# Kernel optimization log

Hardware: AMD Instinct MI355X
Metric: run time of the kernel (lower is better)

Reference implementation:

```python
import jax, jax.numpy as jnp
import numpy as np

B_, S, D = 2, 2048, 2048
F_ = 8192
R = 16
H = 16
HD = D // H
MOD_SCALE = 0.1
EPS = 1e-6


def _rmsnorm(x, w):
    v = jnp.mean(x * x, axis=-1, keepdims=True)
    return x * jax.lax.rsqrt(v + EPS) * w


def setup_inputs() -> dict:
    key = jax.random.key(0)
    ks = jax.random.split(key, 12)
    sd = 0.02
    return {
        "hidden_states": jax.random.normal(ks[0], (B_, S, D), jnp.float32),
        "ln1_w": jnp.ones((D,), jnp.float32),
        "ln2_w": jnp.ones((D,), jnp.float32),
        "Wq": jax.random.normal(ks[1], (D, D), jnp.float32) * sd,
        "Wk": jax.random.normal(ks[2], (D, D), jnp.float32) * sd,
        "Wv": jax.random.normal(ks[3], (D, D), jnp.float32) * sd,
        "Wo": jax.random.normal(ks[4], (D, D), jnp.float32) * sd,
        "A": jax.random.normal(ks[5], (D, R), jnp.float32) * (0.01 / np.sqrt(D)),
        "B": jax.random.normal(ks[6], (R, F_), jnp.float32) * (0.01 / np.sqrt(R)),
        "W_in_base": jax.random.normal(ks[7], (F_, D), jnp.float32) * sd,
        "W_up_base": jax.random.normal(ks[8], (F_, D), jnp.float32) * sd,
        "W_down": jax.random.normal(ks[9], (D, F_), jnp.float32) * sd,
    }


def _attention(x, Wq, Wk, Wv, Wo):
    # x: (b, s, d). Causal multi-head self-attention, torch Linear convention (y = x @ W.T).
    b, s, d = x.shape
    q = (x @ Wq.T).reshape(b, s, H, HD)
    k = (x @ Wk.T).reshape(b, s, H, HD)
    v = (x @ Wv.T).reshape(b, s, H, HD)
    scores = jnp.einsum("bqhd,bkhd->bhqk", q, k) / np.sqrt(HD).astype(np.float32)
    causal = jnp.tril(jnp.ones((s, s), bool))
    scores = jnp.where(causal, scores, jnp.finfo(scores.dtype).min)
    probs = jax.nn.softmax(scores, axis=-1)
    out = jnp.einsum("bhqk,bkhd->bqhd", probs, v).reshape(b, s, d)
    return out @ Wo.T


def reference(hidden_states, ln1_w, ln2_w, Wq, Wk, Wv, Wo, A, B, W_in_base, W_up_base, W_down):
    residual = hidden_states
    x = _rmsnorm(hidden_states, ln1_w)
    attn = _attention(x, Wq, Wk, Wv, Wo)  # (b, s, d)

    # NeuroPlasticComponent: delta_w[b,s,d,f] = sum_r mod[b,s,r] * A[d,r] * B[r,f]
    mod = MOD_SCALE * jnp.tanh(attn @ A)  # (b, s, r)

    # NPT quirk: post_attention_layernorm is applied to the ORIGINAL residual,
    # and attention output is never added into the residual stream.
    h = _rmsnorm(residual, ln2_w)  # (b, s, d)

    # Per-token modulated gate: (W_in_base + delta_w[b,s].T) @ h
    # delta_w[b,s].T @ h = sum_d delta[d,f] h[d] = ((mod * (h @ A)) @ B)[f]
    gate_pre = h @ W_in_base.T + (mod * (h @ A)) @ B  # (b, s, f)
    gate = jax.nn.silu(gate_pre)
    up = h @ W_up_base.T
    mlp_out = (gate * up) @ W_down.T
    return residual + mlp_out
```

## Files before the change

### kernel.cpp

```cpp
#include <hip/hip_runtime.h>

#define DI __device__ __forceinline__

typedef short s16x8 __attribute__((ext_vector_type(8)));
typedef float f32x4 __attribute__((ext_vector_type(4)));

typedef __attribute__((address_space(1))) const unsigned int as1_cuint;
typedef __attribute__((address_space(3))) unsigned int as3_uint;

DI unsigned short f2bf(float f) {
  union { float f; unsigned int u; } v; v.f = f;
  unsigned int r = v.u + 0x7fffu + ((v.u >> 16) & 1u);
  return (unsigned short)(r >> 16);
}
DI float bf2f(unsigned short b) {
  union { unsigned int u; float f; } v; v.u = ((unsigned int)b) << 16;
  return v.f;
}

DI void gl_lds16(const void* g, void* l) {
  __builtin_amdgcn_global_load_lds((as1_cuint*)g, (as3_uint*)l, 16, 0, 0);
}

DI void bar() {
  __builtin_amdgcn_sched_barrier(0);
  __builtin_amdgcn_s_barrier();
  __builtin_amdgcn_sched_barrier(0);
}
DI void s_vmcnt6() { asm volatile("s_waitcnt vmcnt(6)" ::: "memory"); }
DI void s_vmcnt0() { asm volatile("s_waitcnt vmcnt(0)" ::: "memory"); }

DI void stage_half(const unsigned short* gb, size_t r0, int K, int kt,
                   unsigned short* lh, int tid) {
#pragma unroll
  for (int j = 0; j < 2; ++j) {
    int o = j * 8192 + tid * 16;
    int row = o >> 7, cb = o & 127;
    int scb = cb ^ ((row & 7) << 4);
    gl_lds16(gb + (r0 + row) * (size_t)K + kt + (scb >> 1),
             lh + ((j * 8192 + (tid >> 6) * 1024) >> 1));
  }
}

DI s16x8 rd_frag(const unsigned short* lds, int baseE, int rwh, int kh, int lane) {
  int cb = kh * 64 + ((lane >> 4) << 4);
  int scb = cb ^ ((rwh & 7) << 4);
  return *(const s16x8*)&lds[baseE + rwh * 64 + (scb >> 1)];
}

__global__ __launch_bounds__(256) void cvt_f32_bf16(const float* __restrict__ src,
                                                    unsigned short* __restrict__ dst, int n4) {
  int i = blockIdx.x * blockDim.x + threadIdx.x;
  int stride = gridDim.x * blockDim.x;
  for (; i < n4; i += stride) {
    float4 v = ((const float4*)src)[i];
    ((ushort4*)dst)[i] = make_ushort4(f2bf(v.x), f2bf(v.y), f2bf(v.z), f2bf(v.w));
  }
}

__global__ __launch_bounds__(256) void rmsnorm_dual(const float* __restrict__ hs,
                                                    const float* __restrict__ w1,
                                                    const float* __restrict__ w2,
                                                    unsigned short* __restrict__ xo,
                                                    unsigned short* __restrict__ ho) {
  const int D = 2048;
  int t = blockIdx.x, tid = threadIdx.x;
  const float* row = hs + (size_t)t * D;
  float4 a = ((const float4*)row)[tid * 2];
  float4 b = ((const float4*)row)[tid * 2 + 1];
  float ss = a.x * a.x + a.y * a.y + a.z * a.z + a.w * a.w +
             b.x * b.x + b.y * b.y + b.z * b.z + b.w * b.w;
#pragma unroll
  for (int off = 32; off; off >>= 1) ss += __shfl_xor(ss, off);
  __shared__ float red[4];
  int wave = tid >> 6, lane = tid & 63;
  if (lane == 0) red[wave] = ss;
  __syncthreads();
  float tot = red[0] + red[1] + red[2] + red[3];
  float inv = rsqrtf(tot / (float)D + 1e-6f);
  int base = tid * 8;
  float vals[8] = {a.x, a.y, a.z, a.w, b.x, b.y, b.z, b.w};
  float4 w1a = ((const float4*)(w1 + base))[0];
  float4 w1b = ((const float4*)(w1 + base))[1];
  float4 w2a = ((const float4*)(w2 + base))[0];
  float4 w2b = ((const float4*)(w2 + base))[1];
  float w1v[8] = {w1a.x, w1a.y, w1a.z, w1a.w, w1b.x, w1b.y, w1b.z, w1b.w};
  float w2v[8] = {w2a.x, w2a.y, w2a.z, w2a.w, w2b.x, w2b.y, w2b.z, w2b.w};
  unsigned short ox[8], oh[8];
#pragma unroll
  for (int j = 0; j < 8; ++j) {
    float n = vals[j] * inv;
    ox[j] = f2bf(n * w1v[j]);
    oh[j] = f2bf(n * w2v[j]);
  }
  ushort4* xp = (ushort4*)(xo + (size_t)t * D + base);
  ushort4* hp = (ushort4*)(ho + (size_t)t * D + base);
  xp[0] = make_ushort4(ox[0], ox[1], ox[2], ox[3]);
  xp[1] = make_ushort4(ox[4], ox[5], ox[6], ox[7]);
  hp[0] = make_ushort4(oh[0], oh[1], oh[2], oh[3]);
  hp[1] = make_ushort4(oh[4], oh[5], oh[6], oh[7]);
}

#define E_NONE 0
#define E_RES 3

template <int EPI>
__global__ __launch_bounds__(512, 2) void gemm256(
    const unsigned short* __restrict__ Amat, const unsigned short* __restrict__ Bt,
    int N, int K, unsigned short* __restrict__ Cbf, float* __restrict__ Cf,
    const float* __restrict__ Res) {
  __shared__ __align__(16) unsigned short lds[65536];
  int tid = threadIdx.x, lane = tid & 63;
  int w = tid >> 6, wm = w >> 2, wn = w & 3;
  int lr = lane & 15, lkh = lane >> 4;
  int nbn = N >> 8, nwg = gridDim.x, wg = blockIdx.x;
  int cpx = nwg >> 3;
  int swz = (wg & 7) * cpx + (wg >> 3);
  int tm = swz / nbn, tn = swz - tm * nbn;
  size_t m0 = (size_t)tm * 256, n0 = (size_t)tn * 256;
  int NT = K >> 6;

  auto stage = [&](int tau, int slot) {
    if (tau >= NT) return;
    const unsigned short* gb = (slot >= 2) ? Bt : Amat;
    size_t r0 = (slot >= 2) ? (n0 + (size_t)(slot - 2) * 128) : (m0 + (size_t)slot * 128);
    stage_half(gb, r0, K, tau * 64, &lds[(tau & 1) * 32768 + slot * 8192], tid);
  };

  stage(0, 0); stage(0, 2); stage(0, 1); stage(0, 3);
  stage(1, 0); stage(1, 2); stage(1, 1);
  s_vmcnt6();
  bar();

  f32x4 acc[8][4] = {};
  s16x8 afr[4][2], bfr[2][2][2];

  for (int t = 0; t < NT; ++t) {
    int buf = (t & 1) * 32768;
#pragma unroll
    for (int mi = 0; mi < 4; ++mi)
#pragma unroll
      for (int kh = 0; kh < 2; ++kh)
        afr[mi][kh] = rd_frag(lds, buf + 0 * 8192, mi * 32 + wm * 16 + lr, kh, lane);
#pragma unroll
    for (int ni = 0; ni < 2; ++ni)
#pragma unroll
      for (int kh = 0; kh < 2; ++kh)
        bfr[0][ni][kh] = rd_frag(lds, buf + 2 * 8192, ni * 64 + wn * 16 + lr, kh, lane);
    stage(t + 1, 3);
    bar();
    __builtin_amdgcn_s_setprio(1);
#pragma unroll
    for (int mi = 0; mi < 4; ++mi)
#pragma unroll
      for (int ni = 0; ni < 2; ++ni)
#pragma unroll
        for (int kh = 0; kh < 2; ++kh)
          acc[mi][ni] = __builtin_amdgcn_mfma_f32_16x16x32_bf16(afr[mi][kh], bfr[0][ni][kh], acc[mi][ni], 0, 0, 0);
    __builtin_amdgcn_s_setprio(0);
    bar();
#pragma unroll
    for (int ni = 0; ni < 2; ++ni)
#pragma unroll
      for (int kh = 0; kh < 2; ++kh)
        bfr[1][ni][kh] = rd_frag(lds, buf + 3 * 8192, ni * 64 + wn * 16 + lr, kh, lane);
    stage(t + 2, 0);
    bar();
    __builtin_amdgcn_s_setprio(1);
#pragma unroll
    for (int mi = 0; mi < 4; ++mi)
#pragma unroll
      for (int ni = 0; ni < 2; ++ni)
#pragma unroll
        for (int kh = 0; kh < 2; ++kh)
          acc[mi][2 + ni] = __builtin_amdgcn_mfma_f32_16x16x32_bf16(afr[mi][kh], bfr[1][ni][kh], acc[mi][2 + ni], 0, 0, 0);
    __builtin_amdgcn_s_setprio(0);
    bar();
#pragma unroll
    for (int mi = 0; mi < 4; ++mi)
#pragma unroll
      for (int kh = 0; kh < 2; ++kh)
        afr[mi][kh] = rd_frag(lds, buf + 1 * 8192, mi * 32 + wm * 16 + lr, kh, lane);
    stage(t + 2, 2);
    bar();
    __builtin_amdgcn_s_setprio(1);
#pragma unroll
    for (int mi = 0; mi < 4; ++mi)
#pragma unroll
      for (int ni = 0; ni < 2; ++ni)
#pragma unroll
        for (int kh = 0; kh < 2; ++kh)
          acc[4 + mi][ni] = __builtin_amdgcn_mfma_f32_16x16x32_bf16(afr[mi][kh], bfr[0][ni][kh], acc[4 + mi][ni], 0, 0, 0);
    __builtin_amdgcn_s_setprio(0);
    bar();
    stage(t + 2, 1);
    bar();
    __builtin_amdgcn_s_setprio(1);
#pragma unroll
    for (int mi = 0; mi < 4; ++mi)
#pragma unroll
      for (int ni = 0; ni < 2; ++ni)
#pragma unroll
        for (int kh = 0; kh < 2; ++kh)
          acc[4 + mi][2 + ni] = __builtin_amdgcn_mfma_f32_16x16x32_bf16(afr[mi][kh], bfr[1][ni][kh], acc[4 + mi][2 + ni], 0, 0, 0);
    __builtin_amdgcn_s_setprio(0);
    if (t < NT - 2) s_vmcnt6();
    else if (t == NT - 2) s_vmcnt0();
    bar();
  }

#pragma unroll
  for (int mh = 0; mh < 2; ++mh)
#pragma unroll
    for (int mi = 0; mi < 4; ++mi)
#pragma unroll
      for (int r = 0; r < 4; ++r) {
        size_t row = m0 + mh * 128 + mi * 32 + wm * 16 + lkh * 4 + r;
#pragma unroll
        for (int nh = 0; nh < 2; ++nh)
#pragma unroll
          for (int ni = 0; ni < 2; ++ni) {
            size_t col = n0 + nh * 128 + ni * 64 + wn * 16 + lr;
            float v = acc[mh * 4 + mi][nh * 2 + ni][r];
            if constexpr (EPI == E_RES) Cf[row * N + col] = Res[row * N + col] + v;
            else Cbf[row * N + col] = f2bf(v);
          }
      }
}

__global__ __launch_bounds__(512, 2) void gemm_mlp256(
    const unsigned short* __restrict__ Hm, const unsigned short* __restrict__ Wg,
    const unsigned short* __restrict__ Wu,
    const float* __restrict__ cvec, const float* __restrict__ Bsm,
    unsigned short* __restrict__ Out) {
  const int N = 8192, K = 2048, NT = K >> 6;
  __shared__ __align__(16) unsigned short lds[65536];
  int tid = threadIdx.x, lane = tid & 63;
  int w = tid >> 6, wm = w >> 2, wn = w & 3;
  int lr = lane & 15, lkh = lane >> 4;
  int nbn = N >> 7, nwg = gridDim.x, wg = blockIdx.x;
  int cpx = nwg >> 3;
  int swz = (wg & 7) * cpx + (wg >> 3);
  int tm = swz / nbn, tn = swz - tm * nbn;
  size_t m0 = (size_t)tm * 256, n0 = (size_t)tn * 128;

  auto stage = [&](int tau, int slot) {
    if (tau >= NT) return;
    const unsigned short* gb = (slot == 2) ? Wg : (slot == 3) ? Wu : Hm;
    size_t r0 = (slot >= 2) ? n0 : (m0 + (size_t)slot * 128);
    stage_half(gb, r0, K, tau * 64, &lds[(tau & 1) * 32768 + slot * 8192], tid);
  };

  stage(0, 0); stage(0, 2); stage(0, 1); stage(0, 3);
  stage(1, 0); stage(1, 2); stage(1, 1);
  s_vmcnt6();
  bar();

  f32x4 ag[8][2] = {}, au[8][2] = {};
  s16x8 afr[4][2], bg[2][2], bu[2][2];

  for (int t = 0; t < NT; ++t) {
    int buf = (t & 1) * 32768;
#pragma unroll
    for (int mi = 0; mi < 4; ++mi)
#pragma unroll
      for (int kh = 0; kh < 2; ++kh)
        afr[mi][kh] = rd_frag(lds, buf + 0 * 8192, mi * 32 + wm * 16 + lr, kh, lane);
#pragma unroll
    for (int ni = 0; ni < 2; ++ni)
#pragma unroll
      for (int kh = 0; kh < 2; ++kh)
        bg[ni][kh] = rd_frag(lds, buf + 2 * 8192, ni * 64 + wn * 16 + lr, kh, lane);
    stage(t + 1, 3);
    bar();
    __builtin_amdgcn_s_setprio(1);
#pragma unroll
    for (int mi = 0; mi < 4; ++mi)
#pragma unroll
      for (int ni = 0; ni < 2; ++ni)
#pragma unroll
        for (int kh = 0; kh < 2; ++kh)
          ag[mi][ni] = __builtin_amdgcn_mfma_f32_16x16x32_bf16(afr[mi][kh], bg[ni][kh], ag[mi][ni], 0, 0, 0);
    __builtin_amdgcn_s_setprio(0);
    bar();
#pragma unroll
    for (int ni = 0; ni < 2; ++ni)
#pragma unroll
      for (int kh = 0; kh < 2; ++kh)
        bu[ni][kh] = rd_frag(lds, buf + 3 * 8192, ni * 64 + wn * 16 + lr, kh, lane);
    stage(t + 2, 0);
    bar();
    __builtin_amdgcn_s_setprio(1);
#pragma unroll
    for (int mi = 0; mi < 4; ++mi)
#pragma unroll
      for (int ni = 0; ni < 2; ++ni)
#pragma unroll
        for (int kh = 0; kh < 2; ++kh)
          au[mi][ni] = __builtin_amdgcn_mfma_f32_16x16x32_bf16(afr[mi][kh], bu[ni][kh], au[mi][ni], 0, 0, 0);
    __builtin_amdgcn_s_setprio(0);
    bar();
#pragma unroll
    for (int mi = 0; mi < 4; ++mi)
#pragma unroll
      for (int kh = 0; kh < 2; ++kh)
        afr[mi][kh] = rd_frag(lds, buf + 1 * 8192, mi * 32 + wm * 16 + lr, kh, lane);
    stage(t + 2, 2);
    bar();
    __builtin_amdgcn_s_setprio(1);
#pragma unroll
    for (int mi = 0; mi < 4; ++mi)
#pragma unroll
      for (int ni = 0; ni < 2; ++ni)
#pragma unroll
        for (int kh = 0; kh < 2; ++kh)
          ag[4 + mi][ni] = __builtin_amdgcn_mfma_f32_16x16x32_bf16(afr[mi][kh], bg[ni][kh], ag[4 + mi][ni], 0, 0, 0);
    __builtin_amdgcn_s_setprio(0);
    bar();
    stage(t + 2, 1);
    bar();
    __builtin_amdgcn_s_setprio(1);
#pragma unroll
    for (int mi = 0; mi < 4; ++mi)
#pragma unroll
      for (int ni = 0; ni < 2; ++ni)
#pragma unroll
        for (int kh = 0; kh < 2; ++kh)
          au[4 + mi][ni] = __builtin_amdgcn_mfma_f32_16x16x32_bf16(afr[mi][kh], bu[ni][kh], au[4 + mi][ni], 0, 0, 0);
    __builtin_amdgcn_s_setprio(0);
    if (t < NT - 2) s_vmcnt6();
    else if (t == NT - 2) s_vmcnt0();
    bar();
  }

  float* cl = (float*)lds;
  float* bl = (float*)&lds[32768];
#pragma unroll
  for (int j = 0; j < 2; ++j) {
    int fi = tid * 2 + j;
    ((float4*)cl)[fi] = ((const float4*)(cvec + m0 * 16))[fi];
  }
  {
    int fi = tid;
    ((float4*)bl)[fi] = *(const float4*)(Bsm + (size_t)(fi >> 5) * N + n0 + (fi & 31) * 4);
  }
  bar();

#pragma unroll
  for (int mh = 0; mh < 2; ++mh)
#pragma unroll
    for (int mi = 0; mi < 4; ++mi)
#pragma unroll
      for (int r = 0; r < 4; ++r) {
        int rr = mh * 128 + mi * 32 + wm * 16 + lkh * 4 + r;
        size_t row = m0 + rr;
#pragma unroll
        for (int ni = 0; ni < 2; ++ni) {
          int cc = ni * 64 + wn * 16 + lr;
          size_t col = n0 + cc;
          float s = 0.f;
#pragma unroll
          for (int jj = 0; jj < 16; ++jj) s += cl[rr * 16 + jj] * bl[jj * 128 + cc];
          float g = ag[mh * 4 + mi][ni][r] + s;
          float sig = 1.f / (1.f + __expf(-g));
          Out[row * N + col] = f2bf(g * sig * au[mh * 4 + mi][ni][r]);
        }
      }
}

__global__ __launch_bounds__(256) void vtrans(const unsigned short* __restrict__ qkv,
                                              unsigned short* __restrict__ vT) {
  __shared__ unsigned short t[64][72];
  int bh = blockIdx.z, b = bh >> 4, h = bh & 15;
  int k0 = blockIdx.x * 64, d0 = blockIdx.y * 64;
  int tid = threadIdx.x;
#pragma unroll
  for (int j = 0; j < 2; ++j) {
    int idx = tid + j * 256;
    int r = idx >> 3, c8 = (idx & 7) * 8;
    s16x8 v = *(const s16x8*)(qkv + ((size_t)(b * 2048 + k0 + r)) * 6144 + 4096 + h * 128 + d0 + c8);
#pragma unroll
    for (int e = 0; e < 8; ++e) t[r][c8 + e] = (unsigned short)v[e];
  }
  __syncthreads();
#pragma unroll
  for (int j = 0; j < 2; ++j) {
    int idx = tid + j * 256;
    int dr = idx >> 3, k8 = (idx & 7) * 8;
    s16x8 o;
#pragma unroll
    for (int e = 0; e < 8; ++e) o[e] = (short)t[k8 + e][dr];
    *(s16x8*)(vT + (size_t)bh * 262144 + (size_t)(d0 + dr) * 2048 + k0 + k8) = o;
  }
}

__global__ __launch_bounds__(256, 2) void attn_fwd2(const unsigned short* __restrict__ qkv,
                                                    const unsigned short* __restrict__ vT,
                                                    unsigned short* __restrict__ attn) {
  const int LD = 6144;
  __shared__ __align__(16) unsigned short Kt[8192];
  __shared__ __align__(16) unsigned short Vt[8192];
  __shared__ __align__(16) unsigned short Pl[4096];
  int tid = threadIdx.x, w = tid >> 6, lane = tid & 63;
  int lrow = lane & 15, g = lane >> 4;
  int qp = blockIdx.x, bh = blockIdx.y, b = bh >> 4, h = bh & 15;
  const unsigned short* Qb = qkv + (size_t)b * 2048 * LD + h * 128;
  const unsigned short* Kb = Qb + 2048;
  const unsigned short* vTb = vT + (size_t)bh * 262144;
  const float scale = 0.08838834764831845f;

#pragma unroll
  for (int pass = 0; pass < 2; ++pass) {
    int qtile = pass ? (31 - qp) : qp;
    int wq0 = qtile * 64 + w * 16;
    s16x8 qf[4];
#pragma unroll
    for (int kc = 0; kc < 4; ++kc)
      qf[kc] = *(const s16x8*)(Qb + (size_t)(wq0 + lrow) * LD + kc * 32 + g * 8);
    f32x4 ao[8] = {};
    float m_r[4], l_r[4];
#pragma unroll
    for (int r = 0; r < 4; ++r) { m_r[r] = -1e30f; l_r[r] = 0.f; }
    int nkt = qtile + 1;

    for (int kt = 0; kt < nkt; ++kt) {
      int k0 = kt * 64;
      bar();
#pragma unroll
      for (int j = 0; j < 4; ++j) {
        int o = j * 4096 + tid * 16;
        int row = o >> 8, cb = o & 255;
        int scb = cb ^ ((row & 7) << 4);
        gl_lds16(Kb + (size_t)(k0 + row) * LD + (scb >> 1), &Kt[(j * 4096 + w * 1024) >> 1]);
      }
#pragma unroll
      for (int j = 0; j < 4; ++j) {
        int o = j * 4096 + tid * 16;
        int row = o >> 7, cb = o & 127;
        int scb = cb ^ ((row & 7) << 4);
        gl_lds16(vTb + (size_t)row * 2048 + k0 + (scb >> 1), &Vt[(j * 4096 + w * 1024) >> 1]);
      }
      s_vmcnt0();
      bar();
      f32x4 sa[4] = {};
#pragma unroll
      for (int ni = 0; ni < 4; ++ni)
#pragma unroll
        for (int kc = 0; kc < 4; ++kc) {
          int row = ni * 16 + lrow;
          int cb = kc * 64 + g * 16;
          int scb = cb ^ ((row & 7) << 4);
          s16x8 kf = *(const s16x8*)&Kt[row * 128 + (scb >> 1)];
          sa[ni] = __builtin_amdgcn_mfma_f32_16x16x32_bf16(qf[kc], kf, sa[ni], 0, 0, 0);
        }
      if (k0 + 63 > wq0) {
#pragma unroll
        for (int ni = 0; ni < 4; ++ni)
#pragma unroll
          for (int r = 0; r < 4; ++r) {
            int q_idx = wq0 + g * 4 + r, k_idx = k0 + ni * 16 + lrow;
            float sv = sa[ni][r] * scale;
            sa[ni][r] = (k_idx > q_idx) ? -1e30f : sv;
          }
      } else {
#pragma unroll
        for (int ni = 0; ni < 4; ++ni)
#pragma unroll
          for (int r = 0; r < 4; ++r) sa[ni][r] *= scale;
      }
      float mt[4];
#pragma unroll
      for (int r = 0; r < 4; ++r)
        mt[r] = fmaxf(fmaxf(sa[0][r], sa[1][r]), fmaxf(sa[2][r], sa[3][r]));
#pragma unroll
      for (int r = 0; r < 4; ++r)
#pragma unroll
        for (int off = 8; off; off >>= 1) mt[r] = fmaxf(mt[r], __shfl_xor(mt[r], off));
      float al[4];
#pragma unroll
      for (int r = 0; r < 4; ++r) {
        float mn = fmaxf(m_r[r], mt[r]);
        al[r] = __expf(m_r[r] - mn);
        m_r[r] = mn;
      }
      float rs[4] = {0.f, 0.f, 0.f, 0.f};
#pragma unroll
      for (int ni = 0; ni < 4; ++ni)
#pragma unroll
        for (int r = 0; r < 4; ++r) {
          float p = __expf(sa[ni][r] - m_r[r]);
          rs[r] += p;
          int q = g * 4 + r, k = ni * 16 + lrow;
          Pl[w * 1024 + q * 64 + (k ^ ((q & 7) << 3))] = f2bf(p);
        }
#pragma unroll
      for (int r = 0; r < 4; ++r) {
#pragma unroll
        for (int off = 8; off; off >>= 1) rs[r] += __shfl_xor(rs[r], off);
        l_r[r] = l_r[r] * al[r] + rs[r];
      }
#pragma unroll
      for (int df = 0; df < 8; ++df)
#pragma unroll
        for (int r = 0; r < 4; ++r) ao[df][r] *= al[r];
      asm volatile("s_waitcnt lgkmcnt(0)" ::: "memory");
      __builtin_amdgcn_sched_barrier(0);
      s16x8 pa[2];
#pragma unroll
      for (int ks = 0; ks < 2; ++ks)
        pa[ks] = *(const s16x8*)&Pl[w * 1024 + lrow * 64 + ((ks * 32 + g * 8) ^ ((lrow & 7) << 3))];
#pragma unroll
      for (int df = 0; df < 8; ++df) {
#pragma unroll
        for (int ks = 0; ks < 2; ++ks) {
          int row = df * 16 + lrow;
          int cb = ks * 64 + g * 16;
          int scb = cb ^ ((row & 7) << 4);
          s16x8 vf = *(const s16x8*)&Vt[row * 64 + (scb >> 1)];
          ao[df] = __builtin_amdgcn_mfma_f32_16x16x32_bf16(pa[ks], vf, ao[df], 0, 0, 0);
        }
      }
    }
#pragma unroll
    for (int df = 0; df < 8; ++df)
#pragma unroll
      for (int r = 0; r < 4; ++r) {
        int q = wq0 + g * 4 + r;
        float v = ao[df][r] / l_r[r];
        attn[((size_t)b * 2048 + q) * 2048 + h * 128 + df * 16 + lrow] = f2bf(v);
      }
    bar();
  }
}

__global__ __launch_bounds__(256) void modc(const unsigned short* __restrict__ attnO,
                                            const unsigned short* __restrict__ h,
                                            const float* __restrict__ A,
                                            float* __restrict__ cvec) {
  const int D = 2048;
  int t = blockIdx.x * 4 + (threadIdx.x >> 6);
  int lane = threadIdx.x & 63;
  float aA[16] = {}, aH[16] = {};
  for (int i = 0; i < D / 64; ++i) {
    int d = i * 64 + lane;
    float av = bf2f(attnO[(size_t)t * D + d]);
    float hv = bf2f(h[(size_t)t * D + d]);
    const float* ar = A + (size_t)d * 16;
#pragma unroll
    for (int j = 0; j < 16; ++j) {
      float a = ar[j];
      aA[j] += av * a;
      aH[j] += hv * a;
    }
  }
#pragma unroll
  for (int j = 0; j < 16; ++j) {
#pragma unroll
    for (int off = 32; off; off >>= 1) {
      aA[j] += __shfl_xor(aA[j], off);
      aH[j] += __shfl_xor(aH[j], off);
    }
  }
#pragma unroll
  for (int j = 0; j < 16; ++j)
    if (lane == j) cvec[(size_t)t * 16 + j] = 0.1f * tanhf(aA[j]) * aH[j];
}

extern "C" void kernel_launch(void* const* d_in, const int* in_sizes, int n_in,
                              void* d_out, int out_size, void* d_ws, size_t ws_size,
                              hipStream_t stream) {
  const float* hs  = (const float*)d_in[0];
  const float* ln1 = (const float*)d_in[1];
  const float* ln2 = (const float*)d_in[2];
  const float* Wq  = (const float*)d_in[3];
  const float* Wk  = (const float*)d_in[4];
  const float* Wv  = (const float*)d_in[5];
  const float* Wo  = (const float*)d_in[6];
  const float* Am  = (const float*)d_in[7];
  const float* Bm  = (const float*)d_in[8];
  const float* Win = (const float*)d_in[9];
  const float* Wup = (const float*)d_in[10];
  const float* Wdn = (const float*)d_in[11];
  float* out = (float*)d_out;
  (void)in_sizes; (void)n_in;

  const int T = 4096;
  const int Dm = 2048, F = 8192;
  const size_t MB = (size_t)1 << 20;

  const size_t need = 184 * MB;
  if (ws_size < need) {
    hipMemsetAsync(d_out, 0, (size_t)out_size * 4, stream);
    return;
  }
  char* base = (char*)d_ws;
  unsigned short* tb    = (unsigned short*)(base);
  unsigned short* wqkv  = (unsigned short*)(base);
  unsigned short* vT    = (unsigned short*)(base);
  unsigned short* xb    = (unsigned short*)(base + 24 * MB);
  unsigned short* attnO = (unsigned short*)(base + 40 * MB);
  unsigned short* qkv   = (unsigned short*)(base + 64 * MB);
  unsigned short* win   = (unsigned short*)(base + 64 * MB);
  unsigned short* wo    = (unsigned short*)(base + 112 * MB);
  unsigned short* hb    = (unsigned short*)(base + 120 * MB);
  unsigned short* attn  = (unsigned short*)(base + 136 * MB);
  float*          cv    = (float*)(base + 136 * MB);
  unsigned short* wup   = (unsigned short*)(base + 152 * MB);
  unsigned short* wdn   = (unsigned short*)(base + 152 * MB);

  cvt_f32_bf16<<<2048, 256, 0, stream>>>(Wq, wqkv, Dm * Dm / 4);
  cvt_f32_bf16<<<2048, 256, 0, stream>>>(Wk, wqkv + (size_t)Dm * Dm, Dm * Dm / 4);
  cvt_f32_bf16<<<2048, 256, 0, stream>>>(Wv, wqkv + (size_t)2 * Dm * Dm, Dm * Dm / 4);
  cvt_f32_bf16<<<2048, 256, 0, stream>>>(Wo, wo, Dm * Dm / 4);
  rmsnorm_dual<<<T, 256, 0, stream>>>(hs, ln1, ln2, xb, hb);

  gemm256<E_NONE><<<(T / 256) * (3 * Dm / 256), 512, 0, stream>>>(
      xb, wqkv, 3 * Dm, Dm, qkv, nullptr, nullptr);

  vtrans<<<dim3(32, 2, 32), 256, 0, stream>>>(qkv, vT);

  attn_fwd2<<<dim3(16, 32), 256, 0, stream>>>(qkv, vT, attn);

  gemm256<E_NONE><<<(T / 256) * (Dm / 256), 512, 0, stream>>>(
      attn, wo, Dm, Dm, attnO, nullptr, nullptr);

  modc<<<T / 4, 256, 0, stream>>>(attnO, hb, Am, cv);

  cvt_f32_bf16<<<2048, 256, 0, stream>>>(Win, win, F * Dm / 4);
  cvt_f32_bf16<<<2048, 256, 0, stream>>>(Wup, wup, F * Dm / 4);

  gemm_mlp256<<<(T / 256) * (F / 128), 512, 0, stream>>>(hb, win, wup, cv, Bm, tb);

  cvt_f32_bf16<<<2048, 256, 0, stream>>>(Wdn, wdn, Dm * F / 4);
  gemm256<E_RES><<<(T / 256) * (Dm / 256), 512, 0, stream>>>(
      tb, wdn, Dm, F, nullptr, out, hs);
}
```

Before: 905.7 us.

## Switch GEMMs to 256x128 tiles with precomputed LDS offsets and one-stage prefetch

Replaces the 256x256 general GEMM with a 256x128-tile variant, which doubles the workgroup count for the QKV, O-projection and down-projection GEMMs (T=4096 rows). Both the general GEMM and the fused MLP GEMM now precompute swizzled LDS fragment offsets and staging pointers once, instead of recomputing addresses every tile. Both pipelines change from staging two K-tiles ahead to a double-buffered one-tile-ahead prefetch, with fewer barriers per iteration. The smaller tiles lower arithmetic intensity per workgroup, and the shallower prefetch may expose more global-load latency.

```diff
diff --git a/kernel.cpp b/kernel.cpp
--- a/kernel.cpp
+++ b/kernel.cpp
@@ -27,26 +27,12 @@
   __builtin_amdgcn_s_barrier();
   __builtin_amdgcn_sched_barrier(0);
 }
-DI void s_vmcnt6() { asm volatile("s_waitcnt vmcnt(6)" ::: "memory"); }
-DI void s_vmcnt0() { asm volatile("s_waitcnt vmcnt(0)" ::: "memory"); }
-
-DI void stage_half(const unsigned short* gb, size_t r0, int K, int kt,
-                   unsigned short* lh, int tid) {
-#pragma unroll
-  for (int j = 0; j < 2; ++j) {
-    int o = j * 8192 + tid * 16;
-    int row = o >> 7, cb = o & 127;
-    int scb = cb ^ ((row & 7) << 4);
-    gl_lds16(gb + (r0 + row) * (size_t)K + kt + (scb >> 1),
-             lh + ((j * 8192 + (tid >> 6) * 1024) >> 1));
-  }
-}
-
-DI s16x8 rd_frag(const unsigned short* lds, int baseE, int rwh, int kh, int lane) {
-  int cb = kh * 64 + ((lane >> 4) << 4);
-  int scb = cb ^ ((rwh & 7) << 4);
-  return *(const s16x8*)&lds[baseE + rwh * 64 + (scb >> 1)];
-}
+DI void vm0() { asm volatile("s_waitcnt vmcnt(0)" ::: "memory"); }
+DI void vm2() { asm volatile("s_waitcnt vmcnt(2)" ::: "memory"); }
+DI void vm4() { asm volatile("s_waitcnt vmcnt(4)" ::: "memory"); }
+DI void vm6() { asm volatile("s_waitcnt vmcnt(6)" ::: "memory"); }
+
+#define MFMA __builtin_amdgcn_mfma_f32_16x16x32_bf16
 
 __global__ __launch_bounds__(256) void cvt_f32_bf16(const float* __restrict__ src,
                                                     unsigned short* __restrict__ dst, int n4) {
@@ -105,49 +91,71 @@
 #define E_RES 3
 
 template <int EPI>
-__global__ __launch_bounds__(512, 2) void gemm256(
+__global__ __launch_bounds__(512, 2) void gemm_n128(
     const unsigned short* __restrict__ Amat, const unsigned short* __restrict__ Bt,
-    int N, int K, unsigned short* __restrict__ Cbf, float* __restrict__ Cf,
+    int N, int K, int NT,
+    unsigned short* __restrict__ Cbf, float* __restrict__ Cf,
     const float* __restrict__ Res) {
-  __shared__ __align__(16) unsigned short lds[65536];
+  __shared__ __align__(16) unsigned short lds[49152];
   int tid = threadIdx.x, lane = tid & 63;
   int w = tid >> 6, wm = w >> 2, wn = w & 3;
-  int lr = lane & 15, lkh = lane >> 4;
-  int nbn = N >> 8, nwg = gridDim.x, wg = blockIdx.x;
+  int lr = lane & 15, g = lane >> 4;
+  int nbn = N >> 7, nwg = gridDim.x, wg = blockIdx.x;
   int cpx = nwg >> 3;
   int swz = (wg & 7) * cpx + (wg >> 3);
   int tm = swz / nbn, tn = swz - tm * nbn;
-  size_t m0 = (size_t)tm * 256, n0 = (size_t)tn * 256;
-  int NT = K >> 6;
-
-  auto stage = [&](int tau, int slot) {
-    if (tau >= NT) return;
-    const unsigned short* gb = (slot >= 2) ? Bt : Amat;
-    size_t r0 = (slot >= 2) ? (n0 + (size_t)(slot - 2) * 128) : (m0 + (size_t)slot * 128);
-    stage_half(gb, r0, K, tau * 64, &lds[(tau & 1) * 32768 + slot * 8192], tid);
+  size_t m0 = (size_t)tm * 256, n0 = (size_t)tn * 128;
+
+  int boffA[4][2], boffB[2][2];
+#pragma unroll
+  for (int mi = 0; mi < 4; ++mi)
+#pragma unroll
+    for (int kh = 0; kh < 2; ++kh) {
+      int row = mi * 32 + wm * 16 + lr;
+      boffA[mi][kh] = row * 128 + ((kh * 64 + g * 16) ^ ((row & 7) << 4));
+    }
+#pragma unroll
+  for (int ni = 0; ni < 2; ++ni)
+#pragma unroll
+    for (int kh = 0; kh < 2; ++kh) {
+      int row = ni * 64 + wn * 16 + lr;
+      boffB[ni][kh] = row * 128 + ((kh * 64 + g * 16) ^ ((row & 7) << 4));
+    }
+  const char* ldsb = (const char*)lds;
+
+  int srow = tid >> 3;
+  int scb = ((tid & 7) * 16) ^ ((srow & 7) << 4);
+  const unsigned short* pA0 = Amat + (m0 + srow) * (size_t)K + (scb >> 1);
+  const unsigned short* pA1 = pA0 + (size_t)128 * K;
+  const unsigned short* pB  = Bt + (n0 + srow) * (size_t)K + (scb >> 1);
+  const size_t jst = (size_t)64 * K;
+  int dst = w * 512;
+
+  f32x4 acc[8][2] = {};
+
+  auto stg = [&](const unsigned short* p, int BUF, int SLOT) {
+    gl_lds16(p, &lds[BUF * 24576 + SLOT * 8192 + dst]);
+    gl_lds16(p + jst, &lds[BUF * 24576 + SLOT * 8192 + 4096 + dst]);
   };
 
-  stage(0, 0); stage(0, 2); stage(0, 1); stage(0, 3);
-  stage(1, 0); stage(1, 2); stage(1, 1);
-  s_vmcnt6();
+  stg(pA0, 0, 0); stg(pB, 0, 2); stg(pA1, 0, 1);
+  pA0 += 64; pA1 += 64; pB += 64;
+  vm2();
   bar();
 
-  f32x4 acc[8][4] = {};
-  s16x8 afr[4][2], bfr[2][2][2];
-
-  for (int t = 0; t < NT; ++t) {
-    int buf = (t & 1) * 32768;
+  auto tile = [&](int t, int BUF) {
+    s16x8 afr[4][2], bfr[2][2];
 #pragma unroll
     for (int mi = 0; mi < 4; ++mi)
 #pragma unroll
       for (int kh = 0; kh < 2; ++kh)
-        afr[mi][kh] = rd_frag(lds, buf + 0 * 8192, mi * 32 + wm * 16 + lr, kh, lane);
+        afr[mi][kh] = *(const s16x8*)(ldsb + BUF * 49152 + 0 * 16384 + boffA[mi][kh]);
 #pragma unroll
     for (int ni = 0; ni < 2; ++ni)
 #pragma unroll
       for (int kh = 0; kh < 2; ++kh)
-        bfr[0][ni][kh] = rd_frag(lds, buf + 2 * 8192, ni * 64 + wn * 16 + lr, kh, lane);
-    stage(t + 1, 3);
+        bfr[ni][kh] = *(const s16x8*)(ldsb + BUF * 49152 + 2 * 16384 + boffB[ni][kh]);
+    if (t + 1 < NT) { stg(pA0, BUF ^ 1, 0); stg(pB, BUF ^ 1, 2); }
     bar();
     __builtin_amdgcn_s_setprio(1);
 #pragma unroll
@@ -156,15 +164,16 @@
       for (int ni = 0; ni < 2; ++ni)
 #pragma unroll
         for (int kh = 0; kh < 2; ++kh)
-          acc[mi][ni] = __builtin_amdgcn_mfma_f32_16x16x32_bf16(afr[mi][kh], bfr[0][ni][kh], acc[mi][ni], 0, 0, 0);
+          acc[mi][ni] = MFMA(afr[mi][kh], bfr[ni][kh], acc[mi][ni], 0, 0, 0);
     __builtin_amdgcn_s_setprio(0);
-    bar();
-#pragma unroll
-    for (int ni = 0; ni < 2; ++ni)
+    if (t + 1 < NT) vm4(); else vm0();
+    bar();
+#pragma unroll
+    for (int mi = 0; mi < 4; ++mi)
 #pragma unroll
       for (int kh = 0; kh < 2; ++kh)
-        bfr[1][ni][kh] = rd_frag(lds, buf + 3 * 8192, ni * 64 + wn * 16 + lr, kh, lane);
-    stage(t + 2, 0);
+        afr[mi][kh] = *(const s16x8*)(ldsb + BUF * 49152 + 1 * 16384 + boffA[mi][kh]);
+    if (t + 1 < NT) stg(pA1, BUF ^ 1, 1);
     bar();
     __builtin_amdgcn_s_setprio(1);
 #pragma unroll
@@ -173,41 +182,14 @@
       for (int ni = 0; ni < 2; ++ni)
 #pragma unroll
         for (int kh = 0; kh < 2; ++kh)
-          acc[mi][2 + ni] = __builtin_amdgcn_mfma_f32_16x16x32_bf16(afr[mi][kh], bfr[1][ni][kh], acc[mi][2 + ni], 0, 0, 0);
+          acc[4 + mi][ni] = MFMA(afr[mi][kh], bfr[ni][kh], acc[4 + mi][ni], 0, 0, 0);
     __builtin_amdgcn_s_setprio(0);
-    bar();
-#pragma unroll
-    for (int mi = 0; mi < 4; ++mi)
-#pragma unroll
-      for (int kh = 0; kh < 2; ++kh)
-        afr[mi][kh] = rd_frag(lds, buf + 1 * 8192, mi * 32 + wm * 16 + lr, kh, lane);
-    stage(t + 2, 2);
-    bar();
-    __builtin_amdgcn_s_setprio(1);
-#pragma unroll
-    for (int mi = 0; mi < 4; ++mi)
-#pragma unroll
-      for (int ni = 0; ni < 2; ++ni)
-#pragma unroll
-        for (int kh = 0; kh < 2; ++kh)
-          acc[4 + mi][ni] = __builtin_amdgcn_mfma_f32_16x16x32_bf16(afr[mi][kh], bfr[0][ni][kh], acc[4 + mi][ni], 0, 0, 0);
-    __builtin_amdgcn_s_setprio(0);
-    bar();
-    stage(t + 2, 1);
-    bar();
-    __builtin_amdgcn_s_setprio(1);
-#pragma unroll
-    for (int mi = 0; mi < 4; ++mi)
-#pragma unroll
-      for (int ni = 0; ni < 2; ++ni)
-#pragma unroll
-        for (int kh = 0; kh < 2; ++kh)
-          acc[4 + mi][2 + ni] = __builtin_amdgcn_mfma_f32_16x16x32_bf16(afr[mi][kh], bfr[1][ni][kh], acc[4 + mi][2 + ni], 0, 0, 0);
-    __builtin_amdgcn_s_setprio(0);
-    if (t < NT - 2) s_vmcnt6();
-    else if (t == NT - 2) s_vmcnt0();
-    bar();
-  }
+    if (t + 1 < NT) vm2();
+    bar();
+    pA0 += 64; pA1 += 64; pB += 64;
+  };
+
+  for (int t = 0; t < NT; t += 2) { tile(t, 0); tile(t + 1, 1); }
 
 #pragma unroll
   for (int mh = 0; mh < 2; ++mh)
@@ -215,16 +197,14 @@
     for (int mi = 0; mi < 4; ++mi)
 #pragma unroll
       for (int r = 0; r < 4; ++r) {
-        size_t row = m0 + mh * 128 + mi * 32 + wm * 16 + lkh * 4 + r;
-#pragma unroll
-        for (int nh = 0; nh < 2; ++nh)
-#pragma unroll
-          for (int ni = 0; ni < 2; ++ni) {
-            size_t col = n0 + nh * 128 + ni * 64 + wn * 16 + lr;
-            float v = acc[mh * 4 + mi][nh * 2 + ni][r];
-            if constexpr (EPI == E_RES) Cf[row * N + col] = Res[row * N + col] + v;
-            else Cbf[row * N + col] = f2bf(v);
-          }
+        size_t row = m0 + mh * 128 + mi * 32 + wm * 16 + g * 4 + r;
+#pragma unroll
+        for (int ni = 0; ni < 2; ++ni) {
+          size_t col = n0 + ni * 64 + wn * 16 + lr;
+          float v = acc[mh * 4 + mi][ni][r];
+          if constexpr (EPI == E_RES) Cf[row * N + col] = Res[row * N + col] + v;
+          else Cbf[row * N + col] = f2bf(v);
+        }
       }
 }
 
@@ -233,45 +213,68 @@
     const unsigned short* __restrict__ Wu,
     const float* __restrict__ cvec, const float* __restrict__ Bsm,
     unsigned short* __restrict__ Out) {
-  const int N = 8192, K = 2048, NT = K >> 6;
+  const int N = 8192, K = 2048, NT = 32;
   __shared__ __align__(16) unsigned short lds[65536];
   int tid = threadIdx.x, lane = tid & 63;
   int w = tid >> 6, wm = w >> 2, wn = w & 3;
-  int lr = lane & 15, lkh = lane >> 4;
+  int lr = lane & 15, g = lane >> 4;
   int nbn = N >> 7, nwg = gridDim.x, wg = blockIdx.x;
   int cpx = nwg >> 3;
   int swz = (wg & 7) * cpx + (wg >> 3);
   int tm = swz / nbn, tn = swz - tm * nbn;
   size_t m0 = (size_t)tm * 256, n0 = (size_t)tn * 128;
 
-  auto stage = [&](int tau, int slot) {
-    if (tau >= NT) return;
-    const unsigned short* gb = (slot == 2) ? Wg : (slot == 3) ? Wu : Hm;
-    size_t r0 = (slot >= 2) ? n0 : (m0 + (size_t)slot * 128);
-    stage_half(gb, r0, K, tau * 64, &lds[(tau & 1) * 32768 + slot * 8192], tid);
+  int boffA[4][2], boffB[2][2];
+#pragma unroll
+  for (int mi = 0; mi < 4; ++mi)
+#pragma unroll
+    for (int kh = 0; kh < 2; ++kh) {
+      int row = mi * 32 + wm * 16 + lr;
+      boffA[mi][kh] = row * 128 + ((kh * 64 + g * 16) ^ ((row & 7) << 4));
+    }
+#pragma unroll
+  for (int ni = 0; ni < 2; ++ni)
+#pragma unroll
+    for (int kh = 0; kh < 2; ++kh) {
+      int row = ni * 64 + wn * 16 + lr;
+      boffB[ni][kh] = row * 128 + ((kh * 64 + g * 16) ^ ((row & 7) << 4));
+    }
+  const char* ldsb = (const char*)lds;
+
+  int srow = tid >> 3;
+  int scb = ((tid & 7) * 16) ^ ((srow & 7) << 4);
+  const unsigned short* pA0 = Hm + (m0 + srow) * (size_t)K + (scb >> 1);
+  const unsigned short* pA1 = pA0 + (size_t)128 * K;
+  const unsigned short* pBg = Wg + (n0 + srow) * (size_t)K + (scb >> 1);
+  const unsigned short* pBu = Wu + (n0 + srow) * (size_t)K + (scb >> 1);
+  const size_t jst = (size_t)64 * K;
+  int dst = w * 512;
+
+  f32x4 ag[8][2] = {}, au[8][2] = {};
+
+  auto stg = [&](const unsigned short* p, int BUF, int SLOT) {
+    gl_lds16(p, &lds[BUF * 32768 + SLOT * 8192 + dst]);
+    gl_lds16(p + jst, &lds[BUF * 32768 + SLOT * 8192 + 4096 + dst]);
   };
 
-  stage(0, 0); stage(0, 2); stage(0, 1); stage(0, 3);
-  stage(1, 0); stage(1, 2); stage(1, 1);
-  s_vmcnt6();
+  stg(pA0, 0, 0); stg(pBg, 0, 2); stg(pBu, 0, 3); stg(pA1, 0, 1);
+  pA0 += 64; pA1 += 64; pBg += 64; pBu += 64;
+  vm4();
   bar();
 
-  f32x4 ag[8][2] = {}, au[8][2] = {};
-  s16x8 afr[4][2], bg[2][2], bu[2][2];
-
-  for (int t = 0; t < NT; ++t) {
-    int buf = (t & 1) * 32768;
+  auto tile = [&](int t, int BUF) {
+    s16x8 afr[4][2], bg[2][2], bu[2][2];
 #pragma unroll
     for (int mi = 0; mi < 4; ++mi)
 #pragma unroll
       for (int kh = 0; kh < 2; ++kh)
-        afr[mi][kh] = rd_frag(lds, buf + 0 * 8192, mi * 32 + wm * 16 + lr, kh, lane);
+        afr[mi][kh] = *(const s16x8*)(ldsb + BUF * 65536 + 0 * 16384 + boffA[mi][kh]);
 #pragma unroll
     for (int ni = 0; ni < 2; ++ni)
 #pragma unroll
       for (int kh = 0; kh < 2; ++kh)
-        bg[ni][kh] = rd_frag(lds, buf + 2 * 8192, ni * 64 + wn * 16 + lr, kh, lane);
-    stage(t + 1, 3);
+        bg[ni][kh] = *(const s16x8*)(ldsb + BUF * 65536 + 2 * 16384 + boffB[ni][kh]);
+    if (t + 1 < NT) { stg(pA0, BUF ^ 1, 0); stg(pBg, BUF ^ 1, 2); }
     bar();
     __builtin_amdgcn_s_setprio(1);
 #pragma unroll
@@ -280,15 +283,16 @@
       for (int ni = 0; ni < 2; ++ni)
 #pragma unroll
         for (int kh = 0; kh < 2; ++kh)
-          ag[mi][ni] = __builtin_amdgcn_mfma_f32_16x16x32_bf16(afr[mi][kh], bg[ni][kh], ag[mi][ni], 0, 0, 0);
+          ag[mi][ni] = MFMA(afr[mi][kh], bg[ni][kh], ag[mi][ni], 0, 0, 0);
     __builtin_amdgcn_s_setprio(0);
+    if (t + 1 < NT) vm6(); else vm2();
     bar();
 #pragma unroll
     for (int ni = 0; ni < 2; ++ni)
 #pragma unroll
       for (int kh = 0; kh < 2; ++kh)
-        bu[ni][kh] = rd_frag(lds, buf + 3 * 8192, ni * 64 + wn * 16 + lr, kh, lane);
-    stage(t + 2, 0);
+        bu[ni][kh] = *(const s16x8*)(ldsb + BUF * 65536 + 3 * 16384 + boffB[ni][kh]);
+    if (t + 1 < NT) stg(pBu, BUF ^ 1, 3);
     bar();
     __builtin_amdgcn_s_setprio(1);
 #pragma unroll
@@ -297,15 +301,16 @@
       for (int ni = 0; ni < 2; ++ni)
 #pragma unroll
         for (int kh = 0; kh < 2; ++kh)
-          au[mi][ni] = __builtin_amdgcn_mfma_f32_16x16x32_bf16(afr[mi][kh], bu[ni][kh], au[mi][ni], 0, 0, 0);
+          au[mi][ni] = MFMA(afr[mi][kh], bu[ni][kh], au[mi][ni], 0, 0, 0);
     __builtin_amdgcn_s_setprio(0);
+    if (t + 1 < NT) vm6(); else vm0();
     bar();
 #pragma unroll
     for (int mi = 0; mi < 4; ++mi)
 #pragma unroll
       for (int kh = 0; kh < 2; ++kh)
-        afr[mi][kh] = rd_frag(lds, buf + 1 * 8192, mi * 32 + wm * 16 + lr, kh, lane);
-    stage(t + 2, 2);
+        afr[mi][kh] = *(const s16x8*)(ldsb + BUF * 65536 + 1 * 16384 + boffA[mi][kh]);
+    if (t + 1 < NT) stg(pA1, BUF ^ 1, 1);
     bar();
     __builtin_amdgcn_s_setprio(1);
 #pragma unroll
@@ -314,11 +319,9 @@
       for (int ni = 0; ni < 2; ++ni)
 #pragma unroll
         for (int kh = 0; kh < 2; ++kh)
-          ag[4 + mi][ni] = __builtin_amdgcn_mfma_f32_16x16x32_bf16(afr[mi][kh], bg[ni][kh], ag[4 + mi][ni], 0, 0, 0);
+          ag[4 + mi][ni] = MFMA(afr[mi][kh], bg[ni][kh], ag[4 + mi][ni], 0, 0, 0);
     __builtin_amdgcn_s_setprio(0);
     bar();
-    stage(t + 2, 1);
-    bar();
     __builtin_amdgcn_s_setprio(1);
 #pragma unroll
     for (int mi = 0; mi < 4; ++mi)
@@ -326,12 +329,14 @@
       for (int ni = 0; ni < 2; ++ni)
 #pragma unroll
         for (int kh = 0; kh < 2; ++kh)
-          au[4 + mi][ni] = __builtin_amdgcn_mfma_f32_16x16x32_bf16(afr[mi][kh], bu[ni][kh], au[4 + mi][ni], 0, 0, 0);
+          au[4 + mi][ni] = MFMA(afr[mi][kh], bu[ni][kh], au[4 + mi][ni], 0, 0, 0);
     __builtin_amdgcn_s_setprio(0);
-    if (t < NT - 2) s_vmcnt6();
-    else if (t == NT - 2) s_vmcnt0();
-    bar();
-  }
+    if (t + 1 < NT) vm4();
+    bar();
+    pA0 += 64; pA1 += 64; pBg += 64; pBu += 64;
+  };
+
+  for (int t = 0; t < NT; t += 2) { tile(t, 0); tile(t + 1, 1); }
 
   float* cl = (float*)lds;
   float* bl = (float*)&lds[32768];
@@ -352,7 +357,7 @@
     for (int mi = 0; mi < 4; ++mi)
 #pragma unroll
       for (int r = 0; r < 4; ++r) {
-        int rr = mh * 128 + mi * 32 + wm * 16 + lkh * 4 + r;
+        int rr = mh * 128 + mi * 32 + wm * 16 + g * 4 + r;
         size_t row = m0 + rr;
 #pragma unroll
         for (int ni = 0; ni < 2; ++ni) {
@@ -361,9 +366,9 @@
           float s = 0.f;
 #pragma unroll
           for (int jj = 0; jj < 16; ++jj) s += cl[rr * 16 + jj] * bl[jj * 128 + cc];
-          float g = ag[mh * 4 + mi][ni][r] + s;
-          float sig = 1.f / (1.f + __expf(-g));
-          Out[row * N + col] = f2bf(g * sig * au[mh * 4 + mi][ni][r]);
+          float gg = ag[mh * 4 + mi][ni][r] + s;
+          float sig = 1.f / (1.f + __expf(-gg));
+          Out[row * N + col] = f2bf(gg * sig * au[mh * 4 + mi][ni][r]);
         }
       }
 }
@@ -440,7 +445,7 @@
         int scb = cb ^ ((row & 7) << 4);
         gl_lds16(vTb + (size_t)row * 2048 + k0 + (scb >> 1), &Vt[(j * 4096 + w * 1024) >> 1]);
       }
-      s_vmcnt0();
+      vm0();
       bar();
       f32x4 sa[4] = {};
 #pragma unroll
@@ -451,7 +456,7 @@
           int cb = kc * 64 + g * 16;
           int scb = cb ^ ((row & 7) << 4);
           s16x8 kf = *(const s16x8*)&Kt[row * 128 + (scb >> 1)];
-          sa[ni] = __builtin_amdgcn_mfma_f32_16x16x32_bf16(qf[kc], kf, sa[ni], 0, 0, 0);
+          sa[ni] = MFMA(qf[kc], kf, sa[ni], 0, 0, 0);
         }
       if (k0 + 63 > wq0) {
 #pragma unroll
@@ -517,7 +522,7 @@
           int cb = ks * 64 + g * 16;
           int scb = cb ^ ((row & 7) << 4);
           s16x8 vf = *(const s16x8*)&Vt[row * 64 + (scb >> 1)];
-          ao[df] = __builtin_amdgcn_mfma_f32_16x16x32_bf16(pa[ks], vf, ao[df], 0, 0, 0);
+          ao[df] = MFMA(pa[ks], vf, ao[df], 0, 0, 0);
         }
       }
     }
@@ -614,15 +619,14 @@
   cvt_f32_bf16<<<2048, 256, 0, stream>>>(Wo, wo, Dm * Dm / 4);
   rmsnorm_dual<<<T, 256, 0, stream>>>(hs, ln1, ln2, xb, hb);
 
-  gemm256<E_NONE><<<(T / 256) * (3 * Dm / 256), 512, 0, stream>>>(
-      xb, wqkv, 3 * Dm, Dm, qkv, nullptr, nullptr);
+  gemm_n128<E_NONE><<<(T / 256) * (3 * Dm / 128), 512, 0, stream>>>(
+      xb, wqkv, 3 * Dm, Dm, Dm / 64, qkv, nullptr, nullptr);
 
   vtrans<<<dim3(32, 2, 32), 256, 0, stream>>>(qkv, vT);
-
   attn_fwd2<<<dim3(16, 32), 256, 0, stream>>>(qkv, vT, attn);
 
-  gemm256<E_NONE><<<(T / 256) * (Dm / 256), 512, 0, stream>>>(
-      attn, wo, Dm, Dm, attnO, nullptr, nullptr);
+  gemm_n128<E_NONE><<<(T / 256) * (Dm / 128), 512, 0, stream>>>(
+      attn, wo, Dm, Dm, Dm / 64, attnO, nullptr, nullptr);
 
   modc<<<T / 4, 256, 0, stream>>>(attnO, hb, Am, cv);
 
@@ -632,6 +636,6 @@
   gemm_mlp256<<<(T / 256) * (F / 128), 512, 0, stream>>>(hb, win, wup, cv, Bm, tb);
 
   cvt_f32_bf16<<<2048, 256, 0, stream>>>(Wdn, wdn, Dm * F / 4);
-  gemm256<E_RES><<<(T / 256) * (Dm / 256), 512, 0, stream>>>(
-      tb, wdn, Dm, F, nullptr, out, hs);
-}
+  gemm_n128<E_RES><<<(T / 256) * (Dm / 128), 512, 0, stream>>>(
+      tb, wdn, Dm, F, F / 64, nullptr, out, hs);
+}
```

After: 792.0 us. 1.14x faster.
